# Kernel tuning notes

Hardware: AMD Instinct MI355X
Metric: run time of the kernel (lower is better)

Reference implementation:

```python
import jax, jax.numpy as jnp
import numpy as np

N_SI, N_M, N_INT, E = 100000, 100000, 500000, 500000
D_SI, D_M, D_INT, H1, H2 = 128, 128, 64, 32, 16


def _seg_mean(x_src, src, dst, n_dst):
    # gather src features per edge, scatter-mean into dst nodes
    msg = x_src[src]                                                  # [E, d]
    s = jax.ops.segment_sum(msg, dst, num_segments=n_dst)             # [n_dst, d]
    cnt = jax.ops.segment_sum(jnp.ones((src.shape[0],), x_src.dtype), dst,
                              num_segments=n_dst)
    return s / jnp.maximum(cnt, 1.0)[:, None]


def _sage(x_src, x_dst, src, dst, Wl, Wr, b):
    # PyG SAGEConv: lin_l(mean_aggr) + lin_r(x_dst); bias lives in lin_l
    return _seg_mean(x_src, src, dst, x_dst.shape[0]) @ Wl + b + x_dst @ Wr


def setup_inputs() -> dict:
    key = jax.random.key(0)
    ks = jax.random.split(key, 40)
    f = lambda i, shape: jax.random.normal(ks[i], shape, dtype=jnp.float32)
    w = lambda i, shape: 0.1 * jax.random.normal(ks[i], shape, dtype=jnp.float32)
    inp = {
        'x_si': f(0, (N_SI, D_SI)),
        'x_m': f(1, (N_M, D_M)),
        'x_int': f(2, (N_INT, D_INT)),
        # layer 1 SAGEConv params per relation (Wl: src->out, Wr: dst->out)
        'W1l_si2i': w(3, (D_SI, H1)), 'W1r_si2i': w(4, (D_INT, H1)), 'b1_si2i': w(5, (H1,)),
        'W1l_m2i': w(6, (D_M, H1)), 'W1r_m2i': w(7, (D_INT, H1)), 'b1_m2i': w(8, (H1,)),
        'W1l_si': w(9, (D_SI, H1)), 'W1r_si': w(10, (D_SI, H1)), 'b1_si': w(11, (H1,)),
        'W1l_m': w(12, (D_M, H1)), 'W1r_m': w(13, (D_M, H1)), 'b1_m': w(14, (H1,)),
        # layer 2
        'W2l_si2i': w(15, (H1, H2)), 'W2r_si2i': w(16, (H1, H2)), 'b2_si2i': w(17, (H2,)),
        'W2l_m2i': w(18, (H1, H2)), 'W2r_m2i': w(19, (H1, H2)), 'b2_m2i': w(20, (H2,)),
        'W2l_si': w(21, (H1, H2)), 'W2r_si': w(22, (H1, H2)), 'b2_si': w(23, (H2,)),
        'W2l_m': w(24, (H1, H2)), 'W2r_m': w(25, (H1, H2)), 'b2_m': w(26, (H2,)),
        # final linear
        'Wlin': w(27, (H2, 1)), 'blin': w(28, (1,)),
        # edge lists
        'src_si2i': jax.random.randint(ks[29], (E,), 0, N_SI, dtype=jnp.int32),
        'dst_si2i': jax.random.randint(ks[30], (E,), 0, N_INT, dtype=jnp.int32),
        'src_m2i': jax.random.randint(ks[31], (E,), 0, N_M, dtype=jnp.int32),
        'dst_m2i': jax.random.randint(ks[32], (E,), 0, N_INT, dtype=jnp.int32),
        'sl_si': jnp.arange(N_SI, dtype=jnp.int32),
        'sl_m': jnp.arange(N_M, dtype=jnp.int32),
    }
    return inp


def reference(x_si, x_m, x_int,
              W1l_si2i, W1r_si2i, b1_si2i, W1l_m2i, W1r_m2i, b1_m2i,
              W1l_si, W1r_si, b1_si, W1l_m, W1r_m, b1_m,
              W2l_si2i, W2r_si2i, b2_si2i, W2l_m2i, W2r_m2i, b2_m2i,
              W2l_si, W2r_si, b2_si, W2l_m, W2r_m, b2_m,
              Wlin, blin,
              src_si2i, dst_si2i, src_m2i, dst_m2i, sl_si, sl_m):
    # ---- HeteroConv layer 1 (aggr='mean' across relations per dst type) ----
    h_int = 0.5 * (_sage(x_si, x_int, src_si2i, dst_si2i, W1l_si2i, W1r_si2i, b1_si2i)
                   + _sage(x_m, x_int, src_m2i, dst_m2i, W1l_m2i, W1r_m2i, b1_m2i))
    h_si = _sage(x_si, x_si, sl_si, sl_si, W1l_si, W1r_si, b1_si)
    h_m = _sage(x_m, x_m, sl_m, sl_m, W1l_m, W1r_m, b1_m)
    # ReLU; dropout is identity in eval mode
    h_int, h_si, h_m = jax.nn.relu(h_int), jax.nn.relu(h_si), jax.nn.relu(h_m)
    # ---- HeteroConv layer 2 ----
    h_int2 = 0.5 * (_sage(h_si, h_int, src_si2i, dst_si2i, W2l_si2i, W2r_si2i, b2_si2i)
                    + _sage(h_m, h_int, src_m2i, dst_m2i, W2l_m2i, W2r_m2i, b2_m2i))
    # ---- readout on interaction nodes ----
    return (h_int2 @ Wlin + blin)[:, 0]
```

## Files before the change

kernel.cpp:

```cpp
#include <hip/hip_runtime.h>
#include <cstdint>

#define NSI   100000
#define NM    100000
#define NINT  500000
#define NEDGE 500000
#define NB_SCAN 489

static const long OFF_WSI  = 0;
static const long OFF_WM   = 8192;
static const long OFF_WI   = 16384;
static const long OFF_USI  = 18432;
static const long OFF_UM   = 18464;
static const long OFF_V    = 18496;
static const long OFF_C0   = 18528;
static const long OFF_BI   = 18560;
static const long OFF_PSI  = 18592;
static const long OFF_PM   = OFF_PSI + 3200000;
static const long OFF_SSI  = OFF_PM + 3200000;
static const long OFF_SM   = OFF_SSI + 100000;
static const long OFF_RI   = OFF_SM + 100000;
static const long OFF_DEG  = OFF_RI + 16000000;
static const long OFF_RP   = OFF_DEG + 1000000;
static const long OFF_EI   = OFF_RP + 1000064;
static const long OFF_BS   = OFF_EI + 1000000;
static const long OFF_END  = OFF_BS + 1024;

__global__ __launch_bounds__(256) void prep_kernel(
    const float* __restrict__ W1l_si2i, const float* __restrict__ W1l_si, const float* __restrict__ W1r_si,
    const float* __restrict__ W1l_m2i,  const float* __restrict__ W1l_m,  const float* __restrict__ W1r_m,
    const float* __restrict__ W1r_si2i, const float* __restrict__ W1r_m2i,
    const float* __restrict__ b1_si2i,  const float* __restrict__ b1_m2i,
    const float* __restrict__ W2l_si2i, const float* __restrict__ W2l_m2i,
    const float* __restrict__ W2r_si2i, const float* __restrict__ W2r_m2i,
    const float* __restrict__ b2_si2i,  const float* __restrict__ b2_m2i,
    const float* __restrict__ Wlin,     const float* __restrict__ blin,
    float* __restrict__ Wsi, float* __restrict__ Wm, float* __restrict__ Wi, float* __restrict__ bi,
    float* __restrict__ u_si, float* __restrict__ u_m, float* __restrict__ v, float* __restrict__ c0,
    int* __restrict__ rp_si, int* __restrict__ rp_m)
{
    const int tid = threadIdx.x;
    for (int idx = tid; idx < 128 * 64; idx += 256) {
        int k = idx >> 6, c = idx & 63;
        float a, b;
        if (c < 32) { a = W1l_si2i[k * 32 + c];      b = W1l_m2i[k * 32 + c]; }
        else { int cc = c - 32;
               a = W1l_si[k * 32 + cc] + W1r_si[k * 32 + cc];
               b = W1l_m[k * 32 + cc]  + W1r_m[k * 32 + cc]; }
        Wsi[idx] = a; Wm[idx] = b;
    }
    for (int idx = tid; idx < 64 * 32; idx += 256)
        Wi[idx] = 0.5f * (W1r_si2i[idx] + W1r_m2i[idx]);
    if (tid < 32) {
        bi[tid] = 0.5f * (b1_si2i[tid] + b1_m2i[tid]);
        float us = 0.f, um = 0.f, vv = 0.f;
        for (int k = 0; k < 16; ++k) {
            float wl = Wlin[k];
            us += W2l_si2i[tid * 16 + k] * wl;
            um += W2l_m2i[tid * 16 + k] * wl;
            vv += 0.5f * (W2r_si2i[tid * 16 + k] + W2r_m2i[tid * 16 + k]) * wl;
        }
        u_si[tid] = us; u_m[tid] = um; v[tid] = vv;
    }
    if (tid == 0) {
        float c = blin[0];
        for (int k = 0; k < 16; ++k) c += 0.5f * (b2_si2i[k] + b2_m2i[k]) * Wlin[k];
        c0[0] = c;
        rp_si[NINT] = NEDGE;
        rp_m[NINT]  = NEDGE;
    }
}

__global__ __launch_bounds__(256) void gemm_src(
    const float* __restrict__ X, const float* __restrict__ Wcat, const float* __restrict__ bias,
    const float* __restrict__ u,
    float* __restrict__ P, float* __restrict__ s_out, int N)
{
    __shared__ float xs[64 * 132];
    __shared__ float lw[64 * 64];
    __shared__ float sp[64 * 9];
    const int tid = threadIdx.x;
    const long row_base = (long)blockIdx.x * 64;

    #pragma unroll
    for (int i = 0; i < 8; ++i) {
        int idx = tid + i * 256;
        int r = idx >> 5, k4 = idx & 31;
        long rr = row_base + r;
        float4 val = make_float4(0.f, 0.f, 0.f, 0.f);
        if (rr < N) val = ((const float4*)X)[rr * 32 + k4];
        *(float4*)&xs[r * 132 + k4 * 4] = val;
    }

    const int r0 = tid & 15;
    const int c0 = (tid >> 4) * 4;
    float acc[4][4] = {{0.f}};

    for (int half = 0; half < 2; ++half) {
        __syncthreads();
        #pragma unroll
        for (int i = 0; i < 4; ++i) {
            int idx = tid + i * 256;
            ((float4*)lw)[idx] = ((const float4*)Wcat)[half * 1024 + idx];
        }
        __syncthreads();
        const float* xb = xs + half * 64;
        #pragma unroll 4
        for (int k = 0; k < 64; k += 4) {
            float4 xr[4];
            #pragma unroll
            for (int j = 0; j < 4; ++j)
                xr[j] = *(const float4*)&xb[(r0 + 16 * j) * 132 + k];
            #pragma unroll
            for (int kk = 0; kk < 4; ++kk) {
                float4 wv = *(const float4*)&lw[(k + kk) * 64 + c0];
                #pragma unroll
                for (int j = 0; j < 4; ++j) {
                    float xv = (kk == 0) ? xr[j].x : (kk == 1) ? xr[j].y : (kk == 2) ? xr[j].z : xr[j].w;
                    acc[j][0] = fmaf(xv, wv.x, acc[j][0]);
                    acc[j][1] = fmaf(xv, wv.y, acc[j][1]);
                    acc[j][2] = fmaf(xv, wv.z, acc[j][2]);
                    acc[j][3] = fmaf(xv, wv.w, acc[j][3]);
                }
            }
        }
    }

    #pragma unroll
    for (int j = 0; j < 4; ++j) {
        long rr = row_base + r0 + 16 * j;
        if (c0 < 32) {
            if (rr < N)
                *(float4*)&P[rr * 32 + c0] = make_float4(acc[j][0], acc[j][1], acc[j][2], acc[j][3]);
        } else {
            const int cc = c0 - 32;
            float h0 = fmaxf(acc[j][0] + bias[cc + 0], 0.f);
            float h1 = fmaxf(acc[j][1] + bias[cc + 1], 0.f);
            float h2 = fmaxf(acc[j][2] + bias[cc + 2], 0.f);
            float h3 = fmaxf(acc[j][3] + bias[cc + 3], 0.f);
            float part = h0 * u[cc + 0] + h1 * u[cc + 1] + h2 * u[cc + 2] + h3 * u[cc + 3];
            sp[(r0 + 16 * j) * 9 + (cc >> 2)] = part;
        }
    }
    __syncthreads();
    if (tid < 64) {
        long rr = row_base + tid;
        if (rr < N) {
            float t = 0.f;
            #pragma unroll
            for (int g = 0; g < 8; ++g) t += sp[tid * 9 + g];
            s_out[rr] = t;
        }
    }
}

__global__ __launch_bounds__(128) void gemm_int(
    const float* __restrict__ X, const float* __restrict__ W,
    const float* __restrict__ bi,
    float* __restrict__ R, int N)
{
    __shared__ float xs[64 * 68];
    __shared__ float lw[64 * 32];
    const int tid = threadIdx.x;
    const long row_base = (long)blockIdx.x * 64;

    #pragma unroll
    for (int i = 0; i < 4; ++i)
        ((float4*)lw)[tid + i * 128] = ((const float4*)W)[tid + i * 128];
    #pragma unroll
    for (int i = 0; i < 8; ++i) {
        int idx = tid + i * 128;
        int r = idx >> 4, k4 = idx & 15;
        long rr = row_base + r;
        float4 val = make_float4(0.f, 0.f, 0.f, 0.f);
        if (rr < N) val = ((const float4*)X)[rr * 16 + k4];
        *(float4*)&xs[r * 68 + k4 * 4] = val;
    }
    __syncthreads();

    const int r0 = tid & 15;
    const int c0 = (tid >> 4) * 4;
    float acc[4][4] = {{0.f}};
    #pragma unroll 4
    for (int k = 0; k < 64; k += 4) {
        float4 xr[4];
        #pragma unroll
        for (int j = 0; j < 4; ++j)
            xr[j] = *(const float4*)&xs[(r0 + 16 * j) * 68 + k];
        #pragma unroll
        for (int kk = 0; kk < 4; ++kk) {
            float4 wv = *(const float4*)&lw[(k + kk) * 32 + c0];
            #pragma unroll
            for (int j = 0; j < 4; ++j) {
                float xv = (kk == 0) ? xr[j].x : (kk == 1) ? xr[j].y : (kk == 2) ? xr[j].z : xr[j].w;
                acc[j][0] = fmaf(xv, wv.x, acc[j][0]);
                acc[j][1] = fmaf(xv, wv.y, acc[j][1]);
                acc[j][2] = fmaf(xv, wv.z, acc[j][2]);
                acc[j][3] = fmaf(xv, wv.w, acc[j][3]);
            }
        }
    }
    #pragma unroll
    for (int j = 0; j < 4; ++j) {
        long rr = row_base + r0 + 16 * j;
        if (rr >= N) continue;
        float4 o;
        o.x = acc[j][0] + bi[c0 + 0];
        o.y = acc[j][1] + bi[c0 + 1];
        o.z = acc[j][2] + bi[c0 + 2];
        o.w = acc[j][3] + bi[c0 + 3];
        *(float4*)&R[rr * 32 + c0] = o;
    }
}

__global__ __launch_bounds__(256) void hist_kernel(
    const int* __restrict__ dst_si, const int* __restrict__ dst_m,
    int* __restrict__ deg_si, int* __restrict__ deg_m)
{
    int e = blockIdx.x * 256 + threadIdx.x;
    if (e >= NEDGE) return;
    if (blockIdx.y == 0) atomicAdd(&deg_si[dst_si[e]], 1);
    else                 atomicAdd(&deg_m[dst_m[e]], 1);
}

__global__ __launch_bounds__(256) void scan1_kernel(
    const int* __restrict__ deg_si, const int* __restrict__ deg_m,
    int* __restrict__ rp_si, int* __restrict__ rp_m, int* __restrict__ bsum)
{
    const int rel = blockIdx.y;
    const int* deg = rel ? deg_m : deg_si;
    int* rp = rel ? rp_m : rp_si;
    __shared__ int ls[256];
    const int tid = threadIdx.x;
    const int base = blockIdx.x * 1024 + tid * 4;
    int v[4];
    #pragma unroll
    for (int j = 0; j < 4; ++j) v[j] = (base + j < NINT) ? deg[base + j] : 0;
    int tsum = v[0] + v[1] + v[2] + v[3];
    ls[tid] = tsum;
    __syncthreads();
    for (int off = 1; off < 256; off <<= 1) {
        int t = (tid >= off) ? ls[tid - off] : 0;
        __syncthreads();
        ls[tid] += t;
        __syncthreads();
    }
    int run = ls[tid] - tsum;
    #pragma unroll
    for (int j = 0; j < 4; ++j) {
        if (base + j < NINT) rp[base + j] = run;
        run += v[j];
    }
    if (tid == 255) bsum[rel * 512 + blockIdx.x] = ls[255];
}

__global__ __launch_bounds__(512) void scan2_kernel(int* __restrict__ bsum)
{
    int* bs = bsum + blockIdx.y * 512;
    __shared__ int ls[512];
    const int tid = threadIdx.x;
    int v = (tid < NB_SCAN) ? bs[tid] : 0;
    ls[tid] = v;
    __syncthreads();
    for (int off = 1; off < 512; off <<= 1) {
        int t = (tid >= off) ? ls[tid - off] : 0;
        __syncthreads();
        ls[tid] += t;
        __syncthreads();
    }
    bs[tid] = ls[tid] - v;
}

__global__ __launch_bounds__(256) void scan3_kernel(
    int* __restrict__ rp_si, int* __restrict__ rp_m, const int* __restrict__ bsum)
{
    int i = blockIdx.x * 256 + threadIdx.x;
    if (i >= NINT) return;
    int rel = blockIdx.y;
    int* rp = rel ? rp_m : rp_si;
    rp[i] += bsum[rel * 512 + (i >> 10)];
}

__global__ __launch_bounds__(256) void fill_kernel(
    const int* __restrict__ src_si, const int* __restrict__ dst_si,
    const int* __restrict__ src_m,  const int* __restrict__ dst_m,
    const int* __restrict__ rp_si,  const int* __restrict__ rp_m,
    int* __restrict__ deg_si, int* __restrict__ deg_m,
    int* __restrict__ ei_si,  int* __restrict__ ei_m)
{
    int e = blockIdx.x * 256 + threadIdx.x;
    if (e >= NEDGE) return;
    if (blockIdx.y == 0) {
        int dn = dst_si[e], sn = src_si[e];
        int old = atomicSub(&deg_si[dn], 1);
        ei_si[rp_si[dn] + old - 1] = sn;
    } else {
        int dn = dst_m[e], sn = src_m[e];
        int old = atomicSub(&deg_m[dn], 1);
        ei_m[rp_m[dn] + old - 1] = sn;
    }
}

__global__ __launch_bounds__(256) void final_gather(
    const float* __restrict__ r_int,
    const float* __restrict__ p_si, const float* __restrict__ p_m,
    const float* __restrict__ s_si, const float* __restrict__ s_m,
    const int* __restrict__ rp_si, const int* __restrict__ ei_si,
    const int* __restrict__ rp_m,  const int* __restrict__ ei_m,
    const float* __restrict__ v, const float* __restrict__ c0,
    float* __restrict__ out)
{
    long gid = (long)blockIdx.x * 256 + threadIdx.x;
    long node = gid >> 3;
    int f4 = threadIdx.x & 7;
    if (node >= NINT) return;

    int rs  = rp_si[node], res = rp_si[node + 1];
    int rm  = rp_m[node],  rem = rp_m[node + 1];
    float4 r  = ((const float4*)r_int)[node * 8 + f4];
    float4 vf = ((const float4*)v)[f4];
    int ds = res - rs, dm = rem - rm;

    int sn_s = (ds > 0) ? ei_si[rs] : 0;
    int sn_m = (dm > 0) ? ei_m[rm] : 0;

    float4 ps = ((const float4*)p_si)[(long)sn_s * 8 + f4];
    float4 pm = ((const float4*)p_m)[(long)sn_m * 8 + f4];
    float qs = s_si[sn_s];
    float qm = s_m[sn_m];

    float msk_s = (ds > 0) ? 1.f : 0.f;
    float msk_m = (dm > 0) ? 1.f : 0.f;
    float4 a_si = make_float4(msk_s * ps.x, msk_s * ps.y, msk_s * ps.z, msk_s * ps.w);
    float4 a_m  = make_float4(msk_m * pm.x, msk_m * pm.y, msk_m * pm.z, msk_m * pm.w);
    float ss_si = msk_s * qs;
    float ss_m  = msk_m * qm;

    for (int e = 1; e < ds; ++e) {
        int sn = ei_si[rs + e];
        float4 p = ((const float4*)p_si)[(long)sn * 8 + f4];
        a_si.x += p.x; a_si.y += p.y; a_si.z += p.z; a_si.w += p.w;
        ss_si += s_si[sn];
    }
    for (int e = 1; e < dm; ++e) {
        int sn = ei_m[rm + e];
        float4 p = ((const float4*)p_m)[(long)sn * 8 + f4];
        a_m.x += p.x; a_m.y += p.y; a_m.z += p.z; a_m.w += p.w;
        ss_m += s_m[sn];
    }

    float wsc = 0.5f / fmaxf((float)ds, 1.0f);
    float wmc = 0.5f / fmaxf((float)dm, 1.0f);

    float h0 = fmaxf(r.x + wsc * a_si.x + wmc * a_m.x, 0.f);
    float h1 = fmaxf(r.y + wsc * a_si.y + wmc * a_m.y, 0.f);
    float h2 = fmaxf(r.z + wsc * a_si.z + wmc * a_m.z, 0.f);
    float h3 = fmaxf(r.w + wsc * a_si.w + wmc * a_m.w, 0.f);
    float t = h0 * vf.x + h1 * vf.y + h2 * vf.z + h3 * vf.w;
    t += __shfl_xor(t, 1);
    t += __shfl_xor(t, 2);
    t += __shfl_xor(t, 4);
    if (f4 == 0)
        out[node] = t + wsc * ss_si + wmc * ss_m + c0[0];
}

extern "C" void kernel_launch(void* const* d_in, const int* in_sizes, int n_in,
                              void* d_out, int out_size, void* d_ws, size_t ws_size,
                              hipStream_t stream)
{
    const float* x_si     = (const float*)d_in[0];
    const float* x_m      = (const float*)d_in[1];
    const float* x_int    = (const float*)d_in[2];
    const float* W1l_si2i = (const float*)d_in[3];
    const float* W1r_si2i = (const float*)d_in[4];
    const float* b1_si2i  = (const float*)d_in[5];
    const float* W1l_m2i  = (const float*)d_in[6];
    const float* W1r_m2i  = (const float*)d_in[7];
    const float* b1_m2i   = (const float*)d_in[8];
    const float* W1l_si   = (const float*)d_in[9];
    const float* W1r_si   = (const float*)d_in[10];
    const float* b1_si    = (const float*)d_in[11];
    const float* W1l_m    = (const float*)d_in[12];
    const float* W1r_m    = (const float*)d_in[13];
    const float* b1_m     = (const float*)d_in[14];
    const float* W2l_si2i = (const float*)d_in[15];
    const float* W2r_si2i = (const float*)d_in[16];
    const float* b2_si2i  = (const float*)d_in[17];
    const float* W2l_m2i  = (const float*)d_in[18];
    const float* W2r_m2i  = (const float*)d_in[19];
    const float* b2_m2i   = (const float*)d_in[20];
    const float* Wlin     = (const float*)d_in[27];
    const float* blin     = (const float*)d_in[28];
    const int* src_si2i   = (const int*)d_in[29];
    const int* dst_si2i   = (const int*)d_in[30];
    const int* src_m2i    = (const int*)d_in[31];
    const int* dst_m2i    = (const int*)d_in[32];

    float* ws = (float*)d_ws;
    if (ws_size < (size_t)OFF_END * sizeof(float)) return;

    int* deg_si = (int*)(ws + OFF_DEG);
    int* deg_m  = deg_si + 500000;
    int* rp_si  = (int*)(ws + OFF_RP);
    int* rp_m   = rp_si + 500032;
    int* ei_si  = (int*)(ws + OFF_EI);
    int* ei_m   = ei_si + 500000;
    int* bsum   = (int*)(ws + OFF_BS);

    prep_kernel<<<1, 256, 0, stream>>>(
        W1l_si2i, W1l_si, W1r_si, W1l_m2i, W1l_m, W1r_m,
        W1r_si2i, W1r_m2i, b1_si2i, b1_m2i,
        W2l_si2i, W2l_m2i, W2r_si2i, W2r_m2i,
        b2_si2i, b2_m2i, Wlin, blin,
        ws + OFF_WSI, ws + OFF_WM, ws + OFF_WI, ws + OFF_BI,
        ws + OFF_USI, ws + OFF_UM, ws + OFF_V, ws + OFF_C0,
        rp_si, rp_m);

    hipMemsetAsync(deg_si, 0, 1000000 * sizeof(int), stream);

    dim3 egrid((NEDGE + 255) / 256, 2);
    hist_kernel<<<egrid, 256, 0, stream>>>(dst_si2i, dst_m2i, deg_si, deg_m);
    scan1_kernel<<<dim3(NB_SCAN, 2), 256, 0, stream>>>(deg_si, deg_m, rp_si, rp_m, bsum);
    scan2_kernel<<<dim3(1, 2), 512, 0, stream>>>(bsum);
    scan3_kernel<<<dim3((NINT + 255) / 256, 2), 256, 0, stream>>>(rp_si, rp_m, bsum);
    fill_kernel<<<egrid, 256, 0, stream>>>(src_si2i, dst_si2i, src_m2i, dst_m2i,
                                           rp_si, rp_m, deg_si, deg_m, ei_si, ei_m);

    gemm_src<<<(NSI + 63) / 64, 256, 0, stream>>>(x_si, ws + OFF_WSI, b1_si, ws + OFF_USI,
                                                  ws + OFF_PSI, ws + OFF_SSI, NSI);
    gemm_src<<<(NM  + 63) / 64, 256, 0, stream>>>(x_m,  ws + OFF_WM,  b1_m,  ws + OFF_UM,
                                                  ws + OFF_PM,  ws + OFF_SM,  NM);
    gemm_int<<<(NINT + 63) / 64, 128, 0, stream>>>(x_int, ws + OFF_WI, ws + OFF_BI, ws + OFF_RI, NINT);

    final_gather<<<(NINT * 8) / 256, 256, 0, stream>>>(ws + OFF_RI,
                                                       ws + OFF_PSI, ws + OFF_PM,
                                                       ws + OFF_SSI, ws + OFF_SM,
                                                       rp_si, ei_si,
                                                       rp_m,  ei_m,
                                                       ws + OFF_V, ws + OFF_C0, (float*)d_out);
}
```

Baseline: 593.2 us.

## Retile projection GEMMs to 8x8 register tiles with K-chunked smem staging

Both dense projection kernels now give each thread an 8x8 register tile over a larger row block (256 rows for the source GEMM, 512 for the interaction GEMM) and stage X and W through shared memory in 16-wide K chunks. The two source-node GEMMs are merged into one launch using blockIdx.y to pick the node type. The aim is more FMAs per shared-memory load, less LDS per block, and one fewer launch. The cost is higher register pressure from 64 accumulators per thread and more __syncthreads per block across the K loop.

Result: slower. 699.8 us (+18.0%).

```diff
diff --git a/kernel.cpp b/kernel.cpp
--- a/kernel.cpp
+++ b/kernel.cpp
@@ -71,145 +71,178 @@
     }
 }
 
-__global__ __launch_bounds__(256) void gemm_src(
-    const float* __restrict__ X, const float* __restrict__ Wcat, const float* __restrict__ bias,
-    const float* __restrict__ u,
-    float* __restrict__ P, float* __restrict__ s_out, int N)
-{
-    __shared__ float xs[64 * 132];
-    __shared__ float lw[64 * 64];
-    __shared__ float sp[64 * 9];
+__global__ __launch_bounds__(256, 3) void gemm_src(
+    const float* __restrict__ X_si, const float* __restrict__ X_m,
+    const float* __restrict__ Wsi,  const float* __restrict__ Wm,
+    const float* __restrict__ b_si, const float* __restrict__ b_m,
+    const float* __restrict__ u_si, const float* __restrict__ u_m,
+    float* __restrict__ P_si, float* __restrict__ P_m,
+    float* __restrict__ s_si, float* __restrict__ s_m, int N)
+{
+    const int type = blockIdx.y;
+    const float* __restrict__ X    = type ? X_m  : X_si;
+    const float* __restrict__ Wcat = type ? Wm   : Wsi;
+    const float* __restrict__ bias = type ? b_m  : b_si;
+    const float* __restrict__ u    = type ? u_m  : u_si;
+    float* __restrict__ P     = type ? P_m  : P_si;
+    float* __restrict__ s_out = type ? s_m  : s_si;
+
+    __shared__ float xs[256 * 20];
+    __shared__ float lw[16 * 64];
+    __shared__ float sp[256 * 5];
     const int tid = threadIdx.x;
-    const long row_base = (long)blockIdx.x * 64;
-
-    #pragma unroll
-    for (int i = 0; i < 8; ++i) {
-        int idx = tid + i * 256;
-        int r = idx >> 5, k4 = idx & 31;
-        long rr = row_base + r;
-        float4 val = make_float4(0.f, 0.f, 0.f, 0.f);
-        if (rr < N) val = ((const float4*)X)[rr * 32 + k4];
-        *(float4*)&xs[r * 132 + k4 * 4] = val;
-    }
-
-    const int r0 = tid & 15;
-    const int c0 = (tid >> 4) * 4;
-    float acc[4][4] = {{0.f}};
-
-    for (int half = 0; half < 2; ++half) {
+    const long row_base = (long)blockIdx.x * 256;
+
+    const int r0 = tid & 31;
+    const int cg = tid >> 5;
+    float acc[8][8];
+    #pragma unroll
+    for (int j = 0; j < 8; ++j)
+        #pragma unroll
+        for (int c = 0; c < 8; ++c) acc[j][c] = 0.f;
+
+    for (int s = 0; s < 8; ++s) {
         __syncthreads();
         #pragma unroll
         for (int i = 0; i < 4; ++i) {
             int idx = tid + i * 256;
-            ((float4*)lw)[idx] = ((const float4*)Wcat)[half * 1024 + idx];
-        }
-        __syncthreads();
-        const float* xb = xs + half * 64;
-        #pragma unroll 4
-        for (int k = 0; k < 64; k += 4) {
-            float4 xr[4];
+            int r = idx >> 2, k4 = idx & 3;
+            long rr = row_base + r;
+            float4 val = make_float4(0.f, 0.f, 0.f, 0.f);
+            if (rr < N) val = ((const float4*)X)[rr * 32 + s * 4 + k4];
+            *(float4*)&xs[r * 20 + k4 * 4] = val;
+        }
+        ((float4*)lw)[tid] = ((const float4*)Wcat)[s * 256 + tid];
+        __syncthreads();
+
+        #pragma unroll
+        for (int k = 0; k < 16; k += 4) {
+            float4 xr[8];
             #pragma unroll
-            for (int j = 0; j < 4; ++j)
-                xr[j] = *(const float4*)&xb[(r0 + 16 * j) * 132 + k];
+            for (int j = 0; j < 8; ++j)
+                xr[j] = *(const float4*)&xs[(r0 + 32 * j) * 20 + k];
             #pragma unroll
             for (int kk = 0; kk < 4; ++kk) {
-                float4 wv = *(const float4*)&lw[(k + kk) * 64 + c0];
+                float4 wv0 = *(const float4*)&lw[(k + kk) * 64 + cg * 8];
+                float4 wv1 = *(const float4*)&lw[(k + kk) * 64 + cg * 8 + 4];
                 #pragma unroll
-                for (int j = 0; j < 4; ++j) {
+                for (int j = 0; j < 8; ++j) {
                     float xv = (kk == 0) ? xr[j].x : (kk == 1) ? xr[j].y : (kk == 2) ? xr[j].z : xr[j].w;
-                    acc[j][0] = fmaf(xv, wv.x, acc[j][0]);
-                    acc[j][1] = fmaf(xv, wv.y, acc[j][1]);
-                    acc[j][2] = fmaf(xv, wv.z, acc[j][2]);
-                    acc[j][3] = fmaf(xv, wv.w, acc[j][3]);
+                    acc[j][0] = fmaf(xv, wv0.x, acc[j][0]);
+                    acc[j][1] = fmaf(xv, wv0.y, acc[j][1]);
+                    acc[j][2] = fmaf(xv, wv0.z, acc[j][2]);
+                    acc[j][3] = fmaf(xv, wv0.w, acc[j][3]);
+                    acc[j][4] = fmaf(xv, wv1.x, acc[j][4]);
+                    acc[j][5] = fmaf(xv, wv1.y, acc[j][5]);
+                    acc[j][6] = fmaf(xv, wv1.z, acc[j][6]);
+                    acc[j][7] = fmaf(xv, wv1.w, acc[j][7]);
                 }
             }
         }
     }
 
-    #pragma unroll
-    for (int j = 0; j < 4; ++j) {
-        long rr = row_base + r0 + 16 * j;
-        if (c0 < 32) {
-            if (rr < N)
-                *(float4*)&P[rr * 32 + c0] = make_float4(acc[j][0], acc[j][1], acc[j][2], acc[j][3]);
-        } else {
-            const int cc = c0 - 32;
-            float h0 = fmaxf(acc[j][0] + bias[cc + 0], 0.f);
-            float h1 = fmaxf(acc[j][1] + bias[cc + 1], 0.f);
-            float h2 = fmaxf(acc[j][2] + bias[cc + 2], 0.f);
-            float h3 = fmaxf(acc[j][3] + bias[cc + 3], 0.f);
-            float part = h0 * u[cc + 0] + h1 * u[cc + 1] + h2 * u[cc + 2] + h3 * u[cc + 3];
-            sp[(r0 + 16 * j) * 9 + (cc >> 2)] = part;
+    if (cg < 4) {
+        #pragma unroll
+        for (int j = 0; j < 8; ++j) {
+            long rr = row_base + r0 + 32 * j;
+            if (rr < N) {
+                *(float4*)&P[rr * 32 + cg * 8]     = make_float4(acc[j][0], acc[j][1], acc[j][2], acc[j][3]);
+                *(float4*)&P[rr * 32 + cg * 8 + 4] = make_float4(acc[j][4], acc[j][5], acc[j][6], acc[j][7]);
+            }
+        }
+    } else {
+        const int cc = (cg - 4) * 8;
+        float bb[8], uu[8];
+        #pragma unroll
+        for (int c = 0; c < 8; ++c) { bb[c] = bias[cc + c]; uu[c] = u[cc + c]; }
+        #pragma unroll
+        for (int j = 0; j < 8; ++j) {
+            float part = 0.f;
+            #pragma unroll
+            for (int c = 0; c < 8; ++c)
+                part += fmaxf(acc[j][c] + bb[c], 0.f) * uu[c];
+            sp[(r0 + 32 * j) * 5 + (cg - 4)] = part;
         }
     }
     __syncthreads();
-    if (tid < 64) {
+    {
         long rr = row_base + tid;
-        if (rr < N) {
-            float t = 0.f;
-            #pragma unroll
-            for (int g = 0; g < 8; ++g) t += sp[tid * 9 + g];
-            s_out[rr] = t;
-        }
-    }
-}
-
-__global__ __launch_bounds__(128) void gemm_int(
+        if (rr < N)
+            s_out[rr] = sp[tid * 5 + 0] + sp[tid * 5 + 1] + sp[tid * 5 + 2] + sp[tid * 5 + 3];
+    }
+}
+
+__global__ __launch_bounds__(256, 3) void gemm_int(
     const float* __restrict__ X, const float* __restrict__ W,
     const float* __restrict__ bi,
     float* __restrict__ R, int N)
 {
-    __shared__ float xs[64 * 68];
-    __shared__ float lw[64 * 32];
+    __shared__ float xs[512 * 20];
+    __shared__ float lw[16 * 32];
     const int tid = threadIdx.x;
-    const long row_base = (long)blockIdx.x * 64;
-
-    #pragma unroll
-    for (int i = 0; i < 4; ++i)
-        ((float4*)lw)[tid + i * 128] = ((const float4*)W)[tid + i * 128];
-    #pragma unroll
-    for (int i = 0; i < 8; ++i) {
-        int idx = tid + i * 128;
-        int r = idx >> 4, k4 = idx & 15;
-        long rr = row_base + r;
-        float4 val = make_float4(0.f, 0.f, 0.f, 0.f);
-        if (rr < N) val = ((const float4*)X)[rr * 16 + k4];
-        *(float4*)&xs[r * 68 + k4 * 4] = val;
-    }
-    __syncthreads();
-
-    const int r0 = tid & 15;
-    const int c0 = (tid >> 4) * 4;
-    float acc[4][4] = {{0.f}};
-    #pragma unroll 4
-    for (int k = 0; k < 64; k += 4) {
-        float4 xr[4];
-        #pragma unroll
-        for (int j = 0; j < 4; ++j)
-            xr[j] = *(const float4*)&xs[(r0 + 16 * j) * 68 + k];
-        #pragma unroll
-        for (int kk = 0; kk < 4; ++kk) {
-            float4 wv = *(const float4*)&lw[(k + kk) * 32 + c0];
+    const long row_base = (long)blockIdx.x * 512;
+
+    const int r0 = tid & 63;
+    const int cg = tid >> 6;
+    float acc[8][8];
+    #pragma unroll
+    for (int j = 0; j < 8; ++j)
+        #pragma unroll
+        for (int c = 0; c < 8; ++c) acc[j][c] = 0.f;
+
+    for (int s = 0; s < 4; ++s) {
+        __syncthreads();
+        #pragma unroll
+        for (int i = 0; i < 8; ++i) {
+            int idx = tid + i * 256;
+            int r = idx >> 2, k4 = idx & 3;
+            long rr = row_base + r;
+            float4 val = make_float4(0.f, 0.f, 0.f, 0.f);
+            if (rr < N) val = ((const float4*)X)[rr * 16 + s * 4 + k4];
+            *(float4*)&xs[r * 20 + k4 * 4] = val;
+        }
+        if (tid < 128)
+            ((float4*)lw)[tid] = ((const float4*)W)[s * 128 + tid];
+        __syncthreads();
+
+        #pragma unroll
+        for (int k = 0; k < 16; k += 4) {
+            float4 xr[8];
             #pragma unroll
-            for (int j = 0; j < 4; ++j) {
-                float xv = (kk == 0) ? xr[j].x : (kk == 1) ? xr[j].y : (kk == 2) ? xr[j].z : xr[j].w;
-                acc[j][0] = fmaf(xv, wv.x, acc[j][0]);
-                acc[j][1] = fmaf(xv, wv.y, acc[j][1]);
-                acc[j][2] = fmaf(xv, wv.z, acc[j][2]);
-                acc[j][3] = fmaf(xv, wv.w, acc[j][3]);
+            for (int j = 0; j < 8; ++j)
+                xr[j] = *(const float4*)&xs[(r0 + 64 * j) * 20 + k];
+            #pragma unroll
+            for (int kk = 0; kk < 4; ++kk) {
+                float4 wv0 = *(const float4*)&lw[(k + kk) * 32 + cg * 8];
+                float4 wv1 = *(const float4*)&lw[(k + kk) * 32 + cg * 8 + 4];
+                #pragma unroll
+                for (int j = 0; j < 8; ++j) {
+                    float xv = (kk == 0) ? xr[j].x : (kk == 1) ? xr[j].y : (kk == 2) ? xr[j].z : xr[j].w;
+                    acc[j][0] = fmaf(xv, wv0.x, acc[j][0]);
+                    acc[j][1] = fmaf(xv, wv0.y, acc[j][1]);
+                    acc[j][2] = fmaf(xv, wv0.z, acc[j][2]);
+                    acc[j][3] = fmaf(xv, wv0.w, acc[j][3]);
+                    acc[j][4] = fmaf(xv, wv1.x, acc[j][4]);
+                    acc[j][5] = fmaf(xv, wv1.y, acc[j][5]);
+                    acc[j][6] = fmaf(xv, wv1.z, acc[j][6]);
+                    acc[j][7] = fmaf(xv, wv1.w, acc[j][7]);
+                }
             }
         }
     }
-    #pragma unroll
-    for (int j = 0; j < 4; ++j) {
-        long rr = row_base + r0 + 16 * j;
-        if (rr >= N) continue;
-        float4 o;
-        o.x = acc[j][0] + bi[c0 + 0];
-        o.y = acc[j][1] + bi[c0 + 1];
-        o.z = acc[j][2] + bi[c0 + 2];
-        o.w = acc[j][3] + bi[c0 + 3];
-        *(float4*)&R[rr * 32 + c0] = o;
+
+    float bb[8];
+    #pragma unroll
+    for (int c = 0; c < 8; ++c) bb[c] = bi[cg * 8 + c];
+    #pragma unroll
+    for (int j = 0; j < 8; ++j) {
+        long rr = row_base + r0 + 64 * j;
+        if (rr < N) {
+            *(float4*)&R[rr * 32 + cg * 8]     = make_float4(acc[j][0] + bb[0], acc[j][1] + bb[1],
+                                                             acc[j][2] + bb[2], acc[j][3] + bb[3]);
+            *(float4*)&R[rr * 32 + cg * 8 + 4] = make_float4(acc[j][4] + bb[4], acc[j][5] + bb[5],
+                                                             acc[j][6] + bb[6], acc[j][7] + bb[7]);
+        }
     }
 }
 
@@ -426,11 +459,11 @@
     fill_kernel<<<egrid, 256, 0, stream>>>(src_si2i, dst_si2i, src_m2i, dst_m2i,
                                            rp_si, rp_m, deg_si, deg_m, ei_si, ei_m);
 
-    gemm_src<<<(NSI + 63) / 64, 256, 0, stream>>>(x_si, ws + OFF_WSI, b1_si, ws + OFF_USI,
-                                                  ws + OFF_PSI, ws + OFF_SSI, NSI);
-    gemm_src<<<(NM  + 63) / 64, 256, 0, stream>>>(x_m,  ws + OFF_WM,  b1_m,  ws + OFF_UM,
-                                                  ws + OFF_PM,  ws + OFF_SM,  NM);
-    gemm_int<<<(NINT + 63) / 64, 128, 0, stream>>>(x_int, ws + OFF_WI, ws + OFF_BI, ws + OFF_RI, NINT);
+    gemm_src<<<dim3((NSI + 255) / 256, 2), 256, 0, stream>>>(
+        x_si, x_m, ws + OFF_WSI, ws + OFF_WM, b1_si, b1_m,
+        ws + OFF_USI, ws + OFF_UM,
+        ws + OFF_PSI, ws + OFF_PM, ws + OFF_SSI, ws + OFF_SM, NSI);
+    gemm_int<<<(NINT + 511) / 512, 256, 0, stream>>>(x_int, ws + OFF_WI, ws + OFF_BI, ws + OFF_RI, NINT);
 
     final_gather<<<(NINT * 8) / 256, 256, 0, stream>>>(ws + OFF_RI,
                                                        ws + OFF_PSI, ws + OFF_PM,
```
